# Performance work log

Hardware: AMD Instinct MI355X
Metric: run time of the kernel (lower is better)

The kernel has to match this reference:

```python
import jax, jax.numpy as jnp
import numpy as np

K_CORR = 2048        # num_correspondences (init kwarg)
MAX_CORR = 8192      # static pad size for the variable-length nonzero output
THRES_START = 0.5
THRES_STEP = 0.01


def setup_inputs() -> dict:
    key = jax.random.key(0)
    k1, k2, k3 = jax.random.split(key, 3)
    N = M = 8193  # 8192 superpoints + 1 dustbin
    # shift so exp(scores) is mostly well below the 0.5 starting threshold,
    # making the iterative threshold search actually iterate (as in practice
    # with log-domain OT scores)
    matching_scores = jax.random.normal(k1, (N, M), dtype=jnp.float32) - 5.0
    ref_n2p_scores_c = jax.random.uniform(k2, (N - 1,), dtype=jnp.float32)
    src_n2p_scores_c = jax.random.uniform(k3, (M - 1,), dtype=jnp.float32)
    return {
        "matching_scores": matching_scores,
        "ref_n2p_scores_c": ref_n2p_scores_c,
        "src_n2p_scores_c": src_n2p_scores_c,
    }


def _find_thres(inner, k):
    """Replicates: while count(score[:-1,:-1] > thres) < k: thres -= 0.01."""
    def cond(t):
        return jnp.sum(inner > t) < k
    def body(t):
        return t - jnp.float32(THRES_STEP)
    return jax.lax.while_loop(cond, body, jnp.float32(THRES_START))


def reference(matching_scores, ref_n2p_scores_c, src_n2p_scores_c):
    s = jnp.exp(matching_scores)
    # n2p reweighting of the non-dustbin block, as in the torch in-place update
    inner = s[:-1, :-1] * (ref_n2p_scores_c[:, None] * src_n2p_scores_c[None, :])
    # threshold search is discrete -> not differentiated
    thres = _find_thres(jax.lax.stop_gradient(inner), K_CORR)
    mask = inner > thres
    count = jnp.sum(mask)
    # torch returns variable-length nonzero in row-major order; we pad to MAX_CORR
    r, c = jnp.nonzero(mask, size=MAX_CORR, fill_value=0)
    valid = jnp.arange(MAX_CORR) < count
    corr_scores = jnp.where(valid, inner[r, c], 0.0)
    ref_corr_indices = jnp.where(valid, r, -1)
    src_corr_indices = jnp.where(valid, c, -1)
    return ref_corr_indices, src_corr_indices, corr_scores
```

## Files before the change

kernel.cpp:

```cpp
#include <hip/hip_runtime.h>

#define NROWS 8192
#define NCOLS 8192
#define LD    8193
#define NBINS 64
#define KCORR 2048
#define MAXC  8192
#define CAP   192
#define FCUT_LOG (-2.5257286443082556f)

__device__ __forceinline__ float inner_val(float m, float rr, float sc) {
    float p = rr * sc;
    return expf(m) * p;
}

__global__ void init_kernel(float* __restrict__ out, unsigned* __restrict__ hist,
                            unsigned* __restrict__ candcnt) {
    int i = blockIdx.x * blockDim.x + threadIdx.x;
    if (i < 2 * MAXC)       out[i] = -1.0f;
    else if (i < 3 * MAXC)  out[i] = 0.0f;
    if (i < NBINS) hist[i] = 0u;
    if (i < NROWS) candcnt[i] = 0u;
}

__device__ __forceinline__ void slow_bin(float m, float rr, float sc, int col,
                                         const float* t, unsigned* sub,
                                         unsigned* s_cnt, unsigned* ccol,
                                         float* cval, int use_cand) {
    float v = inner_val(m, rr, sc);
    int g = (int)floorf((0.5f - v) * 100.0f) + 1;
    g = (g < 0) ? 0 : ((g > NBINS) ? NBINS : g);
    while (g < NBINS && t[g] >= v) ++g;
    while (g > 0 && t[g - 1] < v) --g;
    atomicAdd(&sub[g], 1u);
    if (use_cand) {
        unsigned slot = atomicAdd(s_cnt, 1u);
        if (slot < CAP) { ccol[slot] = (unsigned)col; cval[slot] = v; }
    }
}

__global__ __launch_bounds__(256) void hist_kernel(
    const float* __restrict__ ms, const float* __restrict__ refs,
    const float* __restrict__ srcs, unsigned* __restrict__ hist,
    unsigned* __restrict__ rowhistT, int use_rowhist,
    unsigned* __restrict__ candcnt, unsigned* __restrict__ cand_col,
    float* __restrict__ cand_v, int use_cand)
{
    __shared__ float t[NBINS];
    __shared__ unsigned sub[NBINS];
    __shared__ unsigned s_cnt;
    int tid = threadIdx.x;
    if (tid == 0) {
        float tv = 0.5f;
        for (int n = 0; n < NBINS; ++n) { t[n] = tv; tv = tv - 0.01f; }
        s_cnt = 0u;
    }
    if (tid < NBINS) sub[tid] = 0u;
    __syncthreads();

    int row = blockIdx.x;
    float rr = refs[row];
    const float* mrow = ms + (size_t)row * LD;
    unsigned* ccol = cand_col + (size_t)row * CAP;
    float*    cval = cand_v  + (size_t)row * CAP;

    int s = (4 - (row & 3)) & 3;
    if (tid < s) {
        float m = mrow[tid];
        if (m > FCUT_LOG)
            slow_bin(m, rr, srcs[tid], tid, t, sub, &s_cnt, ccol, cval, use_cand);
    }
    const float4* b4 = (const float4*)(mrow + s);
    int nb = (NCOLS - s) >> 2;

    float4 q[8];
    #pragma unroll
    for (int k = 0; k < 8; ++k) {
        int i = tid + 256 * k;
        if (k < 7 || i < nb) q[k] = b4[i];
        else q[k] = make_float4(-1e30f, -1e30f, -1e30f, -1e30f);
    }
    #pragma unroll
    for (int k = 0; k < 8; ++k) {
        int c0 = s + 4 * (tid + 256 * k);
        bool any = (q[k].x > FCUT_LOG) | (q[k].y > FCUT_LOG) |
                   (q[k].z > FCUT_LOG) | (q[k].w > FCUT_LOG);
        if (any) {
            if (q[k].x > FCUT_LOG) slow_bin(q[k].x, rr, srcs[c0 + 0], c0 + 0, t, sub, &s_cnt, ccol, cval, use_cand);
            if (q[k].y > FCUT_LOG) slow_bin(q[k].y, rr, srcs[c0 + 1], c0 + 1, t, sub, &s_cnt, ccol, cval, use_cand);
            if (q[k].z > FCUT_LOG) slow_bin(q[k].z, rr, srcs[c0 + 2], c0 + 2, t, sub, &s_cnt, ccol, cval, use_cand);
            if (q[k].w > FCUT_LOG) slow_bin(q[k].w, rr, srcs[c0 + 3], c0 + 3, t, sub, &s_cnt, ccol, cval, use_cand);
        }
    }
    int done = s + (nb << 2);
    if (tid < NCOLS - done) {
        int c = done + tid;
        float m = mrow[c];
        if (m > FCUT_LOG)
            slow_bin(m, rr, srcs[c], c, t, sub, &s_cnt, ccol, cval, use_cand);
    }
    __syncthreads();

    if (tid < 64) {
        unsigned v = sub[tid];
        unsigned p = v;
        #pragma unroll
        for (int off = 1; off < 64; off <<= 1) {
            unsigned u = __shfl_up(p, off);
            if (tid >= off) p += u;
        }
        unsigned slowtot = __shfl(p, 63);
        if (use_rowhist)
            rowhistT[(size_t)tid * NROWS + row] = (tid == 63) ? (unsigned)NCOLS : p;
        unsigned g = (tid == 63) ? (v + (unsigned)NCOLS - slowtot) : v;
        if (g) atomicAdd(&hist[tid], g);
    } else if (tid == 64 && use_cand) {
        candcnt[row] = s_cnt;
    }
}

__global__ __launch_bounds__(1024) void mid_kernel(
    const unsigned* __restrict__ hist, const unsigned* __restrict__ rowhistT,
    float* __restrict__ thres, unsigned* __restrict__ nstar,
    unsigned* __restrict__ rowoff, int use_rowhist)
{
    __shared__ int s_ns;
    __shared__ unsigned ssum[1024];
    int tid = threadIdx.x;
    if (tid < 64) {
        unsigned h = hist[tid];
        unsigned cum = h;
        #pragma unroll
        for (int off = 1; off < 64; off <<= 1) {
            unsigned u = __shfl_up(cum, off);
            if (tid >= off) cum += u;
        }
        unsigned long long mk = __ballot(cum >= (unsigned)KCORR);
        int nsel = mk ? (int)(__ffsll((unsigned long long)mk) - 1) : (NBINS - 1);
        if (tid == 0) {
            float tv = 0.5f;
            for (int n = 0; n < nsel; ++n) tv = tv - 0.01f;
            *thres = tv;
            *nstar = (unsigned)nsel;
            s_ns = nsel;
        }
    }
    __syncthreads();
    if (!use_rowhist) return;
    int ns = s_ns;
    const unsigned* rc = rowhistT + (size_t)ns * NROWS;
    int r0 = tid * 8;
    unsigned c[8], s = 0;
    #pragma unroll
    for (int k = 0; k < 8; ++k) { c[k] = rc[r0 + k]; s += c[k]; }
    ssum[tid] = s;
    __syncthreads();
    for (int off = 1; off < 1024; off <<= 1) {
        unsigned v = (tid >= off) ? ssum[tid - off] : 0u;
        __syncthreads();
        ssum[tid] += v;
        __syncthreads();
    }
    unsigned excl = ssum[tid] - s;
    #pragma unroll
    for (int k = 0; k < 8; ++k) { rowoff[r0 + k] = excl; excl += c[k]; }
    if (tid == 1023) rowoff[NROWS] = excl;
}

__global__ __launch_bounds__(256) void count2_kernel(
    const float* __restrict__ ms, const float* __restrict__ refs,
    const float* __restrict__ srcs, const float* __restrict__ thresp,
    const unsigned* __restrict__ nstar, unsigned* __restrict__ rowcnt,
    int use_rowhist)
{
    int ns = (int)*nstar;
    if (use_rowhist && !(ns >= 42 && ns < 63)) return;
    __shared__ unsigned tot;
    float th = *thresp;
    for (int r4 = 0; r4 < 4; ++r4) {
        int row = blockIdx.x * 4 + r4;
        if (threadIdx.x == 0) tot = 0;
        __syncthreads();
        float rr = refs[row];
        const float* mrow = ms + (size_t)row * LD;
        unsigned cnt = 0;
        for (int c = threadIdx.x; c < NCOLS; c += 256)
            cnt += (inner_val(mrow[c], rr, srcs[c]) > th) ? 1u : 0u;
        atomicAdd(&tot, cnt);
        __syncthreads();
        if (threadIdx.x == 0) rowcnt[row] = tot;
        __syncthreads();
    }
}

__global__ __launch_bounds__(1024) void scan2_kernel(
    const unsigned* __restrict__ rowcnt, const unsigned* __restrict__ nstar,
    unsigned* __restrict__ rowoff, int use_rowhist)
{
    int ns = (int)*nstar;
    if (use_rowhist && !(ns >= 42 && ns < 63)) return;
    __shared__ unsigned ssum[1024];
    int tid = threadIdx.x;
    int r0 = tid * 8;
    unsigned c[8], s = 0;
    for (int k = 0; k < 8; ++k) { c[k] = rowcnt[r0 + k]; s += c[k]; }
    ssum[tid] = s;
    __syncthreads();
    for (int off = 1; off < 1024; off <<= 1) {
        unsigned v = (tid >= off) ? ssum[tid - off] : 0u;
        __syncthreads();
        ssum[tid] += v;
        __syncthreads();
    }
    unsigned excl = ssum[tid] - s;
    for (int k = 0; k < 8; ++k) { rowoff[r0 + k] = excl; excl += c[k]; }
    if (tid == 1023) rowoff[NROWS] = excl;
}

__global__ __launch_bounds__(256) void cwrite_kernel(
    const float* __restrict__ ms, const float* __restrict__ refs,
    const float* __restrict__ srcs, const float* __restrict__ thresp,
    const unsigned* __restrict__ nstar, const unsigned* __restrict__ rowoff,
    const unsigned* __restrict__ candcnt, const unsigned* __restrict__ cand_col,
    const float* __restrict__ cand_v, float* __restrict__ out, int use_cand)
{
    __shared__ unsigned s_col[4][64];
    __shared__ float    s_val[4][64];
    int tid = threadIdx.x, wv = tid >> 6, lane = tid & 63;
    int row = blockIdx.x * 4 + wv;
    unsigned base = rowoff[row], next = rowoff[row + 1];
    if (base == next || base >= MAXC) return;
    float th = *thresp;
    int ns = (int)*nstar;
    unsigned k = next - base;
    bool full = (!use_cand) || (ns >= 42) || (candcnt[row] > CAP) || (k > 64);

    if (!full) {
        unsigned C = candcnt[row];
        const unsigned* cc = cand_col + (size_t)row * CAP;
        const float*    cv = cand_v  + (size_t)row * CAP;
        unsigned nrun = 0;
        for (unsigned c0 = 0; c0 < C; c0 += 64) {
            unsigned i = c0 + lane;
            bool sel = false; unsigned col = 0; float v = 0.f;
            if (i < C) { col = cc[i]; v = cv[i]; sel = (v > th); }
            unsigned long long mk = __ballot(sel);
            if (sel) {
                unsigned idx = nrun + (unsigned)__popcll(mk & ((1ull << lane) - 1ull));
                if (idx < 64) { s_col[wv][idx] = col; s_val[wv][idx] = v; }
            }
            nrun += (unsigned)__popcll(mk);
        }
        __builtin_amdgcn_s_waitcnt(0);
        __builtin_amdgcn_wave_barrier();
        unsigned kk = (nrun < k) ? nrun : k;
        if (kk > 64) kk = 64;
        if (lane < (int)kk) {
            unsigned mycol = s_col[wv][lane];
            float    myval = s_val[wv][lane];
            unsigned rank = 0;
            for (unsigned j = 0; j < kk; ++j)
                rank += (s_col[wv][j] < mycol) ? 1u : 0u;
            unsigned pos = base + rank;
            if (pos < MAXC) {
                out[pos]            = (float)row;
                out[MAXC + pos]     = (float)mycol;
                out[2 * MAXC + pos] = myval;
            }
        }
        return;
    }

    float rr = refs[row];
    const float* mrow = ms + (size_t)row * LD;
    unsigned running = base;
    for (int c0 = 0; c0 < NCOLS && running < next && running < MAXC; c0 += 64) {
        int col = c0 + lane;
        float v = inner_val(mrow[col], rr, srcs[col]);
        bool pred = v > th;
        unsigned long long mk = __ballot(pred);
        if (pred) {
            unsigned pos = running + (unsigned)__popcll(mk & ((1ull << lane) - 1ull));
            if (pos < MAXC) {
                out[pos]            = (float)row;
                out[MAXC + pos]     = (float)col;
                out[2 * MAXC + pos] = v;
            }
        }
        running += (unsigned)__popcll(mk);
    }
}

extern "C" void kernel_launch(void* const* d_in, const int* in_sizes, int n_in,
                              void* d_out, int out_size, void* d_ws, size_t ws_size,
                              hipStream_t stream) {
    const float* ms  = (const float*)d_in[0];
    const float* ref = (const float*)d_in[1];
    const float* src = (const float*)d_in[2];
    float* out = (float*)d_out;

    char* w = (char*)d_ws;
    unsigned* hist   = (unsigned*)(w);
    float*    thres  = (float*)(w + 256);
    unsigned* nstar  = (unsigned*)(w + 260);
    unsigned* rowcnt = (unsigned*)(w + 512);
    unsigned* rowoff = (unsigned*)(w + 512 + NROWS * 4);
    size_t rh_off = 512 + (size_t)NROWS * 4 + (size_t)(NROWS + 1) * 4;
    rh_off = (rh_off + 255) & ~(size_t)255;
    unsigned* rowhistT = (unsigned*)(w + rh_off);
    size_t cc_off = rh_off + (size_t)NBINS * NROWS * 4;
    unsigned* candcnt  = (unsigned*)(w + cc_off);
    size_t col_off = cc_off + (size_t)NROWS * 4;
    unsigned* cand_col = (unsigned*)(w + col_off);
    size_t cv_off = col_off + (size_t)NROWS * CAP * 4;
    float* cand_v      = (float*)(w + cv_off);
    size_t end_off = cv_off + (size_t)NROWS * CAP * 4;

    int use_rowhist = (ws_size >= cc_off) ? 1 : 0;
    int use_cand    = (ws_size >= end_off) ? 1 : 0;

    init_kernel<<<96, 256, 0, stream>>>(out, hist, candcnt);
    hist_kernel<<<NROWS, 256, 0, stream>>>(ms, ref, src, hist, rowhistT,
                                           use_rowhist, candcnt, cand_col,
                                           cand_v, use_cand);
    mid_kernel<<<1, 1024, 0, stream>>>(hist, rowhistT, thres, nstar, rowoff,
                                       use_rowhist);
    count2_kernel<<<NROWS / 4, 256, 0, stream>>>(ms, ref, src, thres, nstar,
                                                 rowcnt, use_rowhist);
    scan2_kernel<<<1, 1024, 0, stream>>>(rowcnt, nstar, rowoff, use_rowhist);
    cwrite_kernel<<<NROWS / 4, 256, 0, stream>>>(ms, ref, src, thres, nstar,
                                                 rowoff, candcnt, cand_col,
                                                 cand_v, out, use_cand);
}
```

Measured before the change: 410.3 us.

## Process four rows per block with double-buffered loads and deferred candidate binning

The histogram kernel now handles four rows per block. It double-buffers float4 loads across half-rows and first pushes raw (col, m) candidates into shared memory, then does exp and binning in a compact second pass. The per-row transposed histogram is replaced by a separate row-count kernel that counts from the stored candidate values, with an overflow flag that falls back to the full recount. This is meant to cut per-block overhead, improve memory-level parallelism and remove the large rowhistT writes. In exchange it adds a kernel launch and relies on candidate caps not overflowing.

New measurement: 382.7 us. 1.07x faster.

```diff
diff --git a/kernel.cpp b/kernel.cpp
--- a/kernel.cpp
+++ b/kernel.cpp
@@ -7,6 +7,7 @@
 #define KCORR 2048
 #define MAXC  8192
 #define CAP   192
+#define RPB   4
 #define FCUT_LOG (-2.5257286443082556f)
 
 __device__ __forceinline__ float inner_val(float m, float rr, float sc) {
@@ -15,89 +16,119 @@
 }
 
 __global__ void init_kernel(float* __restrict__ out, unsigned* __restrict__ hist,
-                            unsigned* __restrict__ candcnt) {
+                            unsigned* __restrict__ ovfl) {
     int i = blockIdx.x * blockDim.x + threadIdx.x;
     if (i < 2 * MAXC)       out[i] = -1.0f;
     else if (i < 3 * MAXC)  out[i] = 0.0f;
     if (i < NBINS) hist[i] = 0u;
-    if (i < NROWS) candcnt[i] = 0u;
-}
-
-__device__ __forceinline__ void slow_bin(float m, float rr, float sc, int col,
-                                         const float* t, unsigned* sub,
-                                         unsigned* s_cnt, unsigned* ccol,
-                                         float* cval, int use_cand) {
-    float v = inner_val(m, rr, sc);
-    int g = (int)floorf((0.5f - v) * 100.0f) + 1;
-    g = (g < 0) ? 0 : ((g > NBINS) ? NBINS : g);
-    while (g < NBINS && t[g] >= v) ++g;
-    while (g > 0 && t[g - 1] < v) --g;
-    atomicAdd(&sub[g], 1u);
-    if (use_cand) {
-        unsigned slot = atomicAdd(s_cnt, 1u);
-        if (slot < CAP) { ccol[slot] = (unsigned)col; cval[slot] = v; }
-    }
+    if (i == NBINS) *ovfl = 0u;
 }
 
 __global__ __launch_bounds__(256) void hist_kernel(
     const float* __restrict__ ms, const float* __restrict__ refs,
     const float* __restrict__ srcs, unsigned* __restrict__ hist,
-    unsigned* __restrict__ rowhistT, int use_rowhist,
     unsigned* __restrict__ candcnt, unsigned* __restrict__ cand_col,
-    float* __restrict__ cand_v, int use_cand)
+    float* __restrict__ cand_v, unsigned* __restrict__ ovfl, int use_cand)
 {
     __shared__ float t[NBINS];
     __shared__ unsigned sub[NBINS];
-    __shared__ unsigned s_cnt;
+    __shared__ unsigned cnt[RPB];
+    __shared__ uint2 pairs[RPB * CAP];
     int tid = threadIdx.x;
     if (tid == 0) {
         float tv = 0.5f;
         for (int n = 0; n < NBINS; ++n) { t[n] = tv; tv = tv - 0.01f; }
-        s_cnt = 0u;
     }
     if (tid < NBINS) sub[tid] = 0u;
+    if (tid < RPB) cnt[tid] = 0u;
     __syncthreads();
 
-    int row = blockIdx.x;
-    float rr = refs[row];
-    const float* mrow = ms + (size_t)row * LD;
-    unsigned* ccol = cand_col + (size_t)row * CAP;
-    float*    cval = cand_v  + (size_t)row * CAP;
-
-    int s = (4 - (row & 3)) & 3;
-    if (tid < s) {
-        float m = mrow[tid];
-        if (m > FCUT_LOG)
-            slow_bin(m, rr, srcs[tid], tid, t, sub, &s_cnt, ccol, cval, use_cand);
-    }
-    const float4* b4 = (const float4*)(mrow + s);
-    int nb = (NCOLS - s) >> 2;
-
-    float4 q[8];
+    int r0 = blockIdx.x * RPB;
+
+    auto push = [&](int r, int col, float m) {
+        unsigned slot = atomicAdd(&cnt[r], 1u);
+        if (slot < CAP)
+            pairs[r * CAP + slot] = make_uint2((unsigned)col, __float_as_uint(m));
+    };
+    auto issue = [&](int b, float4* dst) {
+        int r = b >> 1, h = b & 1;
+        int row = r0 + r;
+        int s = (4 - (row & 3)) & 3;
+        const float4* p4 = (const float4*)(ms + (size_t)row * LD + s);
+        int nb = (NCOLS - s) >> 2;
+        #pragma unroll
+        for (int k = 0; k < 4; ++k) {
+            int i = h * 1024 + k * 256 + tid;
+            if ((h == 1 && k == 3) ? (i < nb) : true) dst[k] = p4[i];
+            else dst[k] = make_float4(-1e30f, -1e30f, -1e30f, -1e30f);
+        }
+    };
+    auto consume = [&](int b, const float4* src4) {
+        int r = b >> 1, h = b & 1;
+        int s = (4 - ((r0 + r) & 3)) & 3;
+        #pragma unroll
+        for (int k = 0; k < 4; ++k) {
+            float4 q = src4[k];
+            int c0 = s + 4 * (h * 1024 + k * 256 + tid);
+            bool a0 = q.x > FCUT_LOG, a1 = q.y > FCUT_LOG;
+            bool a2 = q.z > FCUT_LOG, a3 = q.w > FCUT_LOG;
+            if (a0 | a1 | a2 | a3) {
+                if (a0) push(r, c0 + 0, q.x);
+                if (a1) push(r, c0 + 1, q.y);
+                if (a2) push(r, c0 + 2, q.z);
+                if (a3) push(r, c0 + 3, q.w);
+            }
+        }
+    };
+
+    float4 buf[2][4];
+    issue(0, buf[0]);
     #pragma unroll
-    for (int k = 0; k < 8; ++k) {
-        int i = tid + 256 * k;
-        if (k < 7 || i < nb) q[k] = b4[i];
-        else q[k] = make_float4(-1e30f, -1e30f, -1e30f, -1e30f);
-    }
-    #pragma unroll
-    for (int k = 0; k < 8; ++k) {
-        int c0 = s + 4 * (tid + 256 * k);
-        bool any = (q[k].x > FCUT_LOG) | (q[k].y > FCUT_LOG) |
-                   (q[k].z > FCUT_LOG) | (q[k].w > FCUT_LOG);
-        if (any) {
-            if (q[k].x > FCUT_LOG) slow_bin(q[k].x, rr, srcs[c0 + 0], c0 + 0, t, sub, &s_cnt, ccol, cval, use_cand);
-            if (q[k].y > FCUT_LOG) slow_bin(q[k].y, rr, srcs[c0 + 1], c0 + 1, t, sub, &s_cnt, ccol, cval, use_cand);
-            if (q[k].z > FCUT_LOG) slow_bin(q[k].z, rr, srcs[c0 + 2], c0 + 2, t, sub, &s_cnt, ccol, cval, use_cand);
-            if (q[k].w > FCUT_LOG) slow_bin(q[k].w, rr, srcs[c0 + 3], c0 + 3, t, sub, &s_cnt, ccol, cval, use_cand);
-        }
-    }
-    int done = s + (nb << 2);
-    if (tid < NCOLS - done) {
-        int c = done + tid;
-        float m = mrow[c];
-        if (m > FCUT_LOG)
-            slow_bin(m, rr, srcs[c], c, t, sub, &s_cnt, ccol, cval, use_cand);
+    for (int b = 0; b < 2 * RPB; ++b) {
+        if (b + 1 < 2 * RPB) issue(b + 1, buf[(b + 1) & 1]);
+        consume(b, buf[b & 1]);
+    }
+
+    if (tid < RPB * 8) {
+        int r = tid >> 3, e = tid & 7;
+        int row = r0 + r;
+        int s = (4 - (row & 3)) & 3;
+        int nb = (NCOLS - s) >> 2;
+        int done = s + 4 * nb;
+        int col = -1;
+        if (e < s) col = e;
+        else if (e - s < NCOLS - done) col = done + (e - s);
+        if (col >= 0) {
+            float m = ms[(size_t)row * LD + col];
+            if (m > FCUT_LOG) push(r, col, m);
+        }
+    }
+    __syncthreads();
+
+    for (int r = 0; r < RPB; ++r) {
+        int row = r0 + r;
+        unsigned C = cnt[r];
+        unsigned Cc = (C < CAP) ? C : CAP;
+        float rr = refs[row];
+        for (unsigned i = tid; i < Cc; i += 256) {
+            uint2 pr = pairs[r * CAP + i];
+            int col = (int)pr.x;
+            float m = __uint_as_float(pr.y);
+            float v = inner_val(m, rr, srcs[col]);
+            int g = (int)floorf((0.5f - v) * 100.0f) + 1;
+            g = (g < 0) ? 0 : ((g > NBINS) ? NBINS : g);
+            while (g < NBINS && t[g] >= v) ++g;
+            while (g > 0 && t[g - 1] < v) --g;
+            atomicAdd(&sub[g], 1u);
+            if (use_cand) {
+                cand_col[(size_t)row * CAP + i] = (unsigned)col;
+                cand_v[(size_t)row * CAP + i]   = v;
+            }
+        }
+        if (tid == 0) {
+            if (use_cand) candcnt[row] = C;
+            if (C > CAP) atomicOr(ovfl, 1u);
+        }
     }
     __syncthreads();
 
@@ -109,23 +140,14 @@
             unsigned u = __shfl_up(p, off);
             if (tid >= off) p += u;
         }
-        unsigned slowtot = __shfl(p, 63);
-        if (use_rowhist)
-            rowhistT[(size_t)tid * NROWS + row] = (tid == 63) ? (unsigned)NCOLS : p;
-        unsigned g = (tid == 63) ? (v + (unsigned)NCOLS - slowtot) : v;
+        unsigned binned = __shfl(p, 63);
+        unsigned g = (tid == 63) ? (v + (unsigned)(RPB * NCOLS) - binned) : v;
         if (g) atomicAdd(&hist[tid], g);
-    } else if (tid == 64 && use_cand) {
-        candcnt[row] = s_cnt;
-    }
-}
-
-__global__ __launch_bounds__(1024) void mid_kernel(
-    const unsigned* __restrict__ hist, const unsigned* __restrict__ rowhistT,
-    float* __restrict__ thres, unsigned* __restrict__ nstar,
-    unsigned* __restrict__ rowoff, int use_rowhist)
-{
-    __shared__ int s_ns;
-    __shared__ unsigned ssum[1024];
+    }
+}
+
+__global__ void mid_kernel(const unsigned* __restrict__ hist,
+                           float* __restrict__ thres, unsigned* __restrict__ nstar) {
     int tid = threadIdx.x;
     if (tid < 64) {
         unsigned h = hist[tid];
@@ -142,39 +164,47 @@
             for (int n = 0; n < nsel; ++n) tv = tv - 0.01f;
             *thres = tv;
             *nstar = (unsigned)nsel;
-            s_ns = nsel;
-        }
-    }
-    __syncthreads();
-    if (!use_rowhist) return;
-    int ns = s_ns;
-    const unsigned* rc = rowhistT + (size_t)ns * NROWS;
-    int r0 = tid * 8;
-    unsigned c[8], s = 0;
+        }
+    }
+}
+
+__global__ __launch_bounds__(256) void rowcnt_kernel(
+    const float* __restrict__ ms, const float* __restrict__ refs,
+    const float* __restrict__ srcs, const float* __restrict__ thresp,
+    const unsigned* __restrict__ nstar, const unsigned* __restrict__ ovfl,
+    const unsigned* __restrict__ candcnt, const float* __restrict__ cand_v,
+    unsigned* __restrict__ rowcnt, int use_cand)
+{
+    int ns = (int)*nstar;
+    if (!(use_cand && ns <= 41 && *ovfl == 0u)) return;
+    int tid = threadIdx.x, wv = tid >> 6, lane = tid & 63;
+    int row = blockIdx.x * 4 + wv;
+    float th = *thresp;
+    unsigned C = candcnt[row];
+    unsigned c = 0;
+    if (C <= CAP) {
+        const float* cv = cand_v + (size_t)row * CAP;
+        for (unsigned i = lane; i < C; i += 64)
+            c += (cv[i] > th) ? 1u : 0u;
+    } else {
+        float rr = refs[row];
+        const float* mrow = ms + (size_t)row * LD;
+        for (int col = lane; col < NCOLS; col += 64)
+            c += (inner_val(mrow[col], rr, srcs[col]) > th) ? 1u : 0u;
+    }
     #pragma unroll
-    for (int k = 0; k < 8; ++k) { c[k] = rc[r0 + k]; s += c[k]; }
-    ssum[tid] = s;
-    __syncthreads();
-    for (int off = 1; off < 1024; off <<= 1) {
-        unsigned v = (tid >= off) ? ssum[tid - off] : 0u;
-        __syncthreads();
-        ssum[tid] += v;
-        __syncthreads();
-    }
-    unsigned excl = ssum[tid] - s;
-    #pragma unroll
-    for (int k = 0; k < 8; ++k) { rowoff[r0 + k] = excl; excl += c[k]; }
-    if (tid == 1023) rowoff[NROWS] = excl;
+    for (int off = 32; off > 0; off >>= 1) c += __shfl_down(c, off);
+    if (lane == 0) rowcnt[row] = c;
 }
 
 __global__ __launch_bounds__(256) void count2_kernel(
     const float* __restrict__ ms, const float* __restrict__ refs,
     const float* __restrict__ srcs, const float* __restrict__ thresp,
-    const unsigned* __restrict__ nstar, unsigned* __restrict__ rowcnt,
-    int use_rowhist)
+    const unsigned* __restrict__ nstar, const unsigned* __restrict__ ovfl,
+    unsigned* __restrict__ rowcnt, int use_cand)
 {
     int ns = (int)*nstar;
-    if (use_rowhist && !(ns >= 42 && ns < 63)) return;
+    if (use_cand && ns <= 41 && *ovfl == 0u) return;
     __shared__ unsigned tot;
     float th = *thresp;
     for (int r4 = 0; r4 < 4; ++r4) {
@@ -183,26 +213,24 @@
         __syncthreads();
         float rr = refs[row];
         const float* mrow = ms + (size_t)row * LD;
-        unsigned cnt = 0;
-        for (int c = threadIdx.x; c < NCOLS; c += 256)
-            cnt += (inner_val(mrow[c], rr, srcs[c]) > th) ? 1u : 0u;
-        atomicAdd(&tot, cnt);
+        unsigned c = 0;
+        for (int col = threadIdx.x; col < NCOLS; col += 256)
+            c += (inner_val(mrow[col], rr, srcs[col]) > th) ? 1u : 0u;
+        atomicAdd(&tot, c);
         __syncthreads();
         if (threadIdx.x == 0) rowcnt[row] = tot;
         __syncthreads();
     }
 }
 
-__global__ __launch_bounds__(1024) void scan2_kernel(
-    const unsigned* __restrict__ rowcnt, const unsigned* __restrict__ nstar,
-    unsigned* __restrict__ rowoff, int use_rowhist)
-{
-    int ns = (int)*nstar;
-    if (use_rowhist && !(ns >= 42 && ns < 63)) return;
+__global__ __launch_bounds__(1024) void scan_kernel(
+    const unsigned* __restrict__ rowcnt, unsigned* __restrict__ rowoff)
+{
     __shared__ unsigned ssum[1024];
     int tid = threadIdx.x;
     int r0 = tid * 8;
     unsigned c[8], s = 0;
+    #pragma unroll
     for (int k = 0; k < 8; ++k) { c[k] = rowcnt[r0 + k]; s += c[k]; }
     ssum[tid] = s;
     __syncthreads();
@@ -213,6 +241,7 @@
         __syncthreads();
     }
     unsigned excl = ssum[tid] - s;
+    #pragma unroll
     for (int k = 0; k < 8; ++k) { rowoff[r0 + k] = excl; excl += c[k]; }
     if (tid == 1023) rowoff[NROWS] = excl;
 }
@@ -220,9 +249,10 @@
 __global__ __launch_bounds__(256) void cwrite_kernel(
     const float* __restrict__ ms, const float* __restrict__ refs,
     const float* __restrict__ srcs, const float* __restrict__ thresp,
-    const unsigned* __restrict__ nstar, const unsigned* __restrict__ rowoff,
-    const unsigned* __restrict__ candcnt, const unsigned* __restrict__ cand_col,
-    const float* __restrict__ cand_v, float* __restrict__ out, int use_cand)
+    const unsigned* __restrict__ nstar, const unsigned* __restrict__ ovfl,
+    const unsigned* __restrict__ rowoff, const unsigned* __restrict__ candcnt,
+    const unsigned* __restrict__ cand_col, const float* __restrict__ cand_v,
+    float* __restrict__ out, int use_cand)
 {
     __shared__ unsigned s_col[4][64];
     __shared__ float    s_val[4][64];
@@ -233,7 +263,8 @@
     float th = *thresp;
     int ns = (int)*nstar;
     unsigned k = next - base;
-    bool full = (!use_cand) || (ns >= 42) || (candcnt[row] > CAP) || (k > 64);
+    bool full = (!use_cand) || (ns >= 42) || (*ovfl != 0u) ||
+                (candcnt[row] > CAP) || (k > 64);
 
     if (!full) {
         unsigned C = candcnt[row];
@@ -303,12 +334,11 @@
     unsigned* hist   = (unsigned*)(w);
     float*    thres  = (float*)(w + 256);
     unsigned* nstar  = (unsigned*)(w + 260);
+    unsigned* ovfl   = (unsigned*)(w + 264);
     unsigned* rowcnt = (unsigned*)(w + 512);
     unsigned* rowoff = (unsigned*)(w + 512 + NROWS * 4);
-    size_t rh_off = 512 + (size_t)NROWS * 4 + (size_t)(NROWS + 1) * 4;
-    rh_off = (rh_off + 255) & ~(size_t)255;
-    unsigned* rowhistT = (unsigned*)(w + rh_off);
-    size_t cc_off = rh_off + (size_t)NBINS * NROWS * 4;
+    size_t cc_off = 512 + (size_t)NROWS * 4 + (size_t)(NROWS + 1) * 4;
+    cc_off = (cc_off + 255) & ~(size_t)255;
     unsigned* candcnt  = (unsigned*)(w + cc_off);
     size_t col_off = cc_off + (size_t)NROWS * 4;
     unsigned* cand_col = (unsigned*)(w + col_off);
@@ -316,19 +346,19 @@
     float* cand_v      = (float*)(w + cv_off);
     size_t end_off = cv_off + (size_t)NROWS * CAP * 4;
 
-    int use_rowhist = (ws_size >= cc_off) ? 1 : 0;
-    int use_cand    = (ws_size >= end_off) ? 1 : 0;
-
-    init_kernel<<<96, 256, 0, stream>>>(out, hist, candcnt);
-    hist_kernel<<<NROWS, 256, 0, stream>>>(ms, ref, src, hist, rowhistT,
-                                           use_rowhist, candcnt, cand_col,
-                                           cand_v, use_cand);
-    mid_kernel<<<1, 1024, 0, stream>>>(hist, rowhistT, thres, nstar, rowoff,
-                                       use_rowhist);
+    int use_cand = (ws_size >= end_off) ? 1 : 0;
+
+    init_kernel<<<96, 256, 0, stream>>>(out, hist, ovfl);
+    hist_kernel<<<NROWS / RPB, 256, 0, stream>>>(ms, ref, src, hist, candcnt,
+                                                 cand_col, cand_v, ovfl, use_cand);
+    mid_kernel<<<1, 64, 0, stream>>>(hist, thres, nstar);
+    rowcnt_kernel<<<NROWS / 4, 256, 0, stream>>>(ms, ref, src, thres, nstar,
+                                                 ovfl, candcnt, cand_v, rowcnt,
+                                                 use_cand);
     count2_kernel<<<NROWS / 4, 256, 0, stream>>>(ms, ref, src, thres, nstar,
-                                                 rowcnt, use_rowhist);
-    scan2_kernel<<<1, 1024, 0, stream>>>(rowcnt, nstar, rowoff, use_rowhist);
+                                                 ovfl, rowcnt, use_cand);
+    scan_kernel<<<1, 1024, 0, stream>>>(rowcnt, rowoff);
     cwrite_kernel<<<NROWS / 4, 256, 0, stream>>>(ms, ref, src, thres, nstar,
-                                                 rowoff, candcnt, cand_col,
+                                                 ovfl, rowoff, candcnt, cand_col,
                                                  cand_v, out, use_cand);
 }
```
